# Performance work log

Hardware: AMD Instinct MI355X
Metric: run time of the kernel (lower is better)

Reference implementation:

```python
import jax, jax.numpy as jnp
import numpy as np

N, D = 32, 16  # output capsules, output capsule dim
J, I = 16, 8   # input capsules, input capsule dim
B = 16384

def setup_inputs() -> dict:
    key = jax.random.key(0)
    k1, k2 = jax.random.split(key)
    inputs = jax.random.normal(k1, (B, J, I), dtype=jnp.float32)
    # kaiming_normal_ on (N,16,8,D): fan_in computed from dims -> std = sqrt(2/fan_in)
    fan_in = I * D  # torch fan_in for a 4D tensor (N,16,8,D) is dim1*receptive? faithful scale: gain*sqrt(1/fan)
    W = jax.random.normal(k2, (N, J, I, D), dtype=jnp.float32) * np.float32(np.sqrt(2.0 / (J * I * D / N if False else fan_in)))
    b = jnp.zeros((N, J, 1), dtype=jnp.float32)
    return {"inputs": inputs, "W": W, "b": b}

def reference(inputs, W, b):
    # pose transform: u[b,n,j,z] = sum_i inputs[b,j,i] * W[n,j,i,z]
    u = jnp.einsum('bji,njiz->bnjz', inputs, W)          # (B, N, J, D)
    # self-agreement: c[b,n,i] = sum_{k,j} u[b,n,i,j] * u[b,n,k,j]
    c = jnp.einsum('bnij,bnj->bni', u, u.sum(axis=-2))   # (B, N, J)
    c = c[..., None] / jnp.sqrt(jnp.float32(D))          # (B, N, J, 1)
    c = jax.nn.softmax(c, axis=1)                        # softmax over N axis (torch dim=1)
    c = c + b                                            # broadcast (N, J, 1)
    s = jnp.sum(u * c, axis=-2)                          # (B, N, D)
    return s
```

## Files before the change

kernel.cpp:

```cpp
#include <hip/hip_runtime.h>

#define B_TOT 16384
#define TBB   16
#define NTH   256
#define SLS   524

typedef short bf16x8 __attribute__((ext_vector_type(8)));
typedef float f32x4  __attribute__((ext_vector_type(4)));
union U4 { bf16x8 v; uint4 q; };

__device__ __forceinline__ unsigned f2bf(float f) {
    unsigned u = __float_as_uint(f);
    return (u + 0x7fffu + ((u >> 16) & 1u)) >> 16;
}

__device__ __forceinline__ uint4 packrow(const float* src) {
    uint4 o;
    o.x = f2bf(src[0])  | (f2bf(src[16])  << 16);
    o.y = f2bf(src[32]) | (f2bf(src[48])  << 16);
    o.z = f2bf(src[64]) | (f2bf(src[80])  << 16);
    o.w = f2bf(src[96]) | (f2bf(src[112]) << 16);
    return o;
}

__global__ void prepack(const float* __restrict__ W, uint4* __restrict__ Wp)
{
    const int t = blockIdx.x * 256 + threadIdx.x;
    if (t < 8192) {
        const int lane = t & 63, s = (t >> 6) & 3, n = t >> 8;
        const int q = lane >> 4, z = lane & 15;
        const int j = 4 * s + q;
        Wp[t] = packrow(W + (size_t)(n * 16 + j) * 128 + z);
    } else {
        const int u = t - 8192;
        const int lane = u & 63, j = (u >> 6) & 15, n = u >> 10;
        const int q = lane >> 4, z = lane & 15;
        uint4 o = make_uint4(0u, 0u, 0u, 0u);
        if (q == (j & 3))
            o = packrow(W + (size_t)(n * 16 + j) * 128 + z);
        Wp[t] = o;
    }
}

__global__ __launch_bounds__(NTH, 4)
void caps(const float* __restrict__ X, const uint4* __restrict__ Wp,
          const float* __restrict__ Bias, float* __restrict__ Out)
{
    __shared__ __align__(16) float sL[TBB * SLS];
    __shared__ float sBias[512];

    const int t    = threadIdx.x;
    const int lane = t & 63;
    const int wv   = t >> 6;
    const int b16  = lane & 15;
    const int q    = lane >> 4;
    const long bb  = (long)blockIdx.x * TBB;

    sBias[t]       = Bias[t];
    sBias[t + 256] = Bias[t + 256];

    uint4 xq[4];
    #pragma unroll
    for (int s = 0; s < 4; ++s) {
        const float* xs = X + (bb + b16) * 128 + (4 * s + q) * 8;
        float4 a = *reinterpret_cast<const float4*>(xs);
        float4 c = *reinterpret_cast<const float4*>(xs + 4);
        uint4 o;
        o.x = f2bf(a.x) | (f2bf(a.y) << 16);
        o.y = f2bf(a.z) | (f2bf(a.w) << 16);
        o.z = f2bf(c.x) | (f2bf(c.y) << 16);
        o.w = f2bf(c.z) | (f2bf(c.w) << 16);
        xq[s] = o;
    }

    const f32x4 zero4 = {0.f, 0.f, 0.f, 0.f};

    #pragma unroll 1
    for (int nq = 0; nq < 8; ++nq) {
        const int n = wv * 8 + nq;
        const uint4* wk = Wp + n * 256 + lane;

        f32x4 usum = zero4;
        #pragma unroll
        for (int s = 0; s < 4; ++s) {
            U4 a;  a.q  = wk[s * 64];
            U4 xb; xb.q = xq[s];
            usum = __builtin_amdgcn_mfma_f32_16x16x32_bf16(a.v, xb.v, usum, 0, 0, 0);
        }

        const uint4* wj = Wp + 8192 + n * 1024 + lane;
        float lv[16];
        #pragma unroll
        for (int j = 0; j < 16; ++j) {
            U4 a;  a.q  = wj[j * 64];
            U4 xb; xb.q = xq[j >> 2];
            f32x4 u = __builtin_amdgcn_mfma_f32_16x16x32_bf16(a.v, xb.v, zero4, 0, 0, 0);
            float p = u[0] * usum[0];
            p = fmaf(u[1], usum[1], p);
            p = fmaf(u[2], usum[2], p);
            p = fmaf(u[3], usum[3], p);
            p += __shfl_xor(p, 16);
            p += __shfl_xor(p, 32);
            lv[j] = p * 0.25f;
        }
        if (lane < 16) {
            float4* dst = reinterpret_cast<float4*>(&sL[b16 * SLS + n * 16]);
            dst[0] = make_float4(lv[0],  lv[1],  lv[2],  lv[3]);
            dst[1] = make_float4(lv[4],  lv[5],  lv[6],  lv[7]);
            dst[2] = make_float4(lv[8],  lv[9],  lv[10], lv[11]);
            dst[3] = make_float4(lv[12], lv[13], lv[14], lv[15]);
        }
    }
    __syncthreads();

    {
        const int sb = t >> 4, sj = t & 15;
        float l[32];
        #pragma unroll
        for (int n = 0; n < 32; ++n) l[n] = sL[sb * SLS + n * 16 + sj];
        float m = l[0];
        #pragma unroll
        for (int n = 1; n < 32; ++n) m = fmaxf(m, l[n]);
        float Z = 0.f;
        #pragma unroll
        for (int n = 0; n < 32; ++n) { l[n] = __expf(l[n] - m); Z += l[n]; }
        const float inv = 1.0f / Z;
        #pragma unroll
        for (int n = 0; n < 32; ++n)
            sL[sb * SLS + n * 16 + sj] = fmaf(l[n], inv, sBias[n * 16 + sj]);
    }
    __syncthreads();

    #pragma unroll 2
    for (int nq = 0; nq < 8; ++nq) {
        const int n = wv * 8 + nq;
        const uint4* wj = Wp + 8192 + n * 1024 + lane;
        float s0 = 0.f, s1 = 0.f, s2 = 0.f, s3 = 0.f;
        #pragma unroll
        for (int jp = 0; jp < 8; ++jp) {
            float2 c2 = *reinterpret_cast<const float2*>(&sL[b16 * SLS + n * 16 + 2 * jp]);
            U4 a0; a0.q = wj[(2 * jp) * 64];
            U4 a1; a1.q = wj[(2 * jp + 1) * 64];
            U4 x0; x0.q = xq[jp >> 1];
            f32x4 u0 = __builtin_amdgcn_mfma_f32_16x16x32_bf16(a0.v, x0.v, zero4, 0, 0, 0);
            f32x4 u1 = __builtin_amdgcn_mfma_f32_16x16x32_bf16(a1.v, x0.v, zero4, 0, 0, 0);
            s0 = fmaf(c2.x, u0[0], s0); s0 = fmaf(c2.y, u1[0], s0);
            s1 = fmaf(c2.x, u0[1], s1); s1 = fmaf(c2.y, u1[1], s1);
            s2 = fmaf(c2.x, u0[2], s2); s2 = fmaf(c2.y, u1[2], s2);
            s3 = fmaf(c2.x, u0[3], s3); s3 = fmaf(c2.y, u1[3], s3);
        }
        float4* op = reinterpret_cast<float4*>(Out + (bb + b16) * 512 + n * 16 + q * 4);
        *op = make_float4(s0, s1, s2, s3);
    }
}

extern "C" void kernel_launch(void* const* d_in, const int* in_sizes, int n_in,
                              void* d_out, int out_size, void* d_ws, size_t ws_size,
                              hipStream_t stream) {
    const float* X  = (const float*)d_in[0];
    const float* W  = (const float*)d_in[1];
    const float* Bi = (const float*)d_in[2];
    float* Out = (float*)d_out;

    uint4* Wp = (uint4*)d_ws;
    prepack<<<160, 256, 0, stream>>>(W, Wp);
    caps<<<B_TOT / TBB, NTH, 0, stream>>>(X, Wp, Bi, Out);
}
```

Measured before the change: 113.8 us.

## Derive per-j masked weight fragments in registers and prefetch next capsule weights

The prepack kernel no longer writes the zero-padded per-j weight copies. The main kernel now builds each per-j MFMA operand by AND-masking the packed 4-row fragment with a lane-group mask, which cuts the weight traffic per block from 1280 to 256 uint4 per capsule. The next capsule's fragments are also prefetched into registers while the current one is computed, in both passes. This costs extra VGPRs and a few ALU ops per MFMA, and the second-pass unroll drops from 2 to 1.

```diff
diff --git a/kernel.cpp b/kernel.cpp
--- a/kernel.cpp
+++ b/kernel.cpp
@@ -26,20 +26,9 @@
 __global__ void prepack(const float* __restrict__ W, uint4* __restrict__ Wp)
 {
     const int t = blockIdx.x * 256 + threadIdx.x;
-    if (t < 8192) {
-        const int lane = t & 63, s = (t >> 6) & 3, n = t >> 8;
-        const int q = lane >> 4, z = lane & 15;
-        const int j = 4 * s + q;
-        Wp[t] = packrow(W + (size_t)(n * 16 + j) * 128 + z);
-    } else {
-        const int u = t - 8192;
-        const int lane = u & 63, j = (u >> 6) & 15, n = u >> 10;
-        const int q = lane >> 4, z = lane & 15;
-        uint4 o = make_uint4(0u, 0u, 0u, 0u);
-        if (q == (j & 3))
-            o = packrow(W + (size_t)(n * 16 + j) * 128 + z);
-        Wp[t] = o;
-    }
+    const int lane = t & 63, s = (t >> 6) & 3, n = t >> 8;
+    const int q = lane >> 4, z = lane & 15;
+    Wp[t] = packrow(W + (size_t)(n * 16 + 4 * s + q) * 128 + z);
 }
 
 __global__ __launch_bounds__(NTH, 4)
@@ -59,6 +48,10 @@
     sBias[t]       = Bias[t];
     sBias[t + 256] = Bias[t + 256];
 
+    unsigned moct[4];
+    #pragma unroll
+    for (int c = 0; c < 4; ++c) moct[c] = (q == c) ? 0xffffffffu : 0u;
+
     uint4 xq[4];
     #pragma unroll
     for (int s = 0; s < 4; ++s) {
@@ -75,24 +68,39 @@
 
     const f32x4 zero4 = {0.f, 0.f, 0.f, 0.f};
 
+    auto maskA = [&](const uint4& wkf, int c) {
+        U4 a;
+        const unsigned m = moct[c];
+        a.q.x = wkf.x & m; a.q.y = wkf.y & m;
+        a.q.z = wkf.z & m; a.q.w = wkf.w & m;
+        return a;
+    };
+
+    uint4 wk[4], wn[4];
+
+    {
+        const uint4* p0 = Wp + (wv * 8) * 256 + lane;
+        wk[0] = p0[0]; wk[1] = p0[64]; wk[2] = p0[128]; wk[3] = p0[192];
+    }
     #pragma unroll 1
     for (int nq = 0; nq < 8; ++nq) {
-        const int n = wv * 8 + nq;
-        const uint4* wk = Wp + n * 256 + lane;
+        const int n  = wv * 8 + nq;
+        const int np = (nq < 7) ? n + 1 : n;
+        const uint4* pn = Wp + np * 256 + lane;
+        wn[0] = pn[0]; wn[1] = pn[64]; wn[2] = pn[128]; wn[3] = pn[192];
 
         f32x4 usum = zero4;
         #pragma unroll
         for (int s = 0; s < 4; ++s) {
-            U4 a;  a.q  = wk[s * 64];
+            U4 a;  a.q  = wk[s];
             U4 xb; xb.q = xq[s];
             usum = __builtin_amdgcn_mfma_f32_16x16x32_bf16(a.v, xb.v, usum, 0, 0, 0);
         }
 
-        const uint4* wj = Wp + 8192 + n * 1024 + lane;
         float lv[16];
         #pragma unroll
         for (int j = 0; j < 16; ++j) {
-            U4 a;  a.q  = wj[j * 64];
+            U4 a  = maskA(wk[j >> 2], j & 3);
             U4 xb; xb.q = xq[j >> 2];
             f32x4 u = __builtin_amdgcn_mfma_f32_16x16x32_bf16(a.v, xb.v, zero4, 0, 0, 0);
             float p = u[0] * usum[0];
@@ -110,6 +118,7 @@
             dst[2] = make_float4(lv[8],  lv[9],  lv[10], lv[11]);
             dst[3] = make_float4(lv[12], lv[13], lv[14], lv[15]);
         }
+        wk[0] = wn[0]; wk[1] = wn[1]; wk[2] = wn[2]; wk[3] = wn[3];
     }
     __syncthreads();
 
@@ -131,16 +140,23 @@
     }
     __syncthreads();
 
-    #pragma unroll 2
+    {
+        const uint4* p0 = Wp + (wv * 8) * 256 + lane;
+        wk[0] = p0[0]; wk[1] = p0[64]; wk[2] = p0[128]; wk[3] = p0[192];
+    }
+    #pragma unroll 1
     for (int nq = 0; nq < 8; ++nq) {
-        const int n = wv * 8 + nq;
-        const uint4* wj = Wp + 8192 + n * 1024 + lane;
+        const int n  = wv * 8 + nq;
+        const int np = (nq < 7) ? n + 1 : n;
+        const uint4* pn = Wp + np * 256 + lane;
+        wn[0] = pn[0]; wn[1] = pn[64]; wn[2] = pn[128]; wn[3] = pn[192];
+
         float s0 = 0.f, s1 = 0.f, s2 = 0.f, s3 = 0.f;
         #pragma unroll
         for (int jp = 0; jp < 8; ++jp) {
             float2 c2 = *reinterpret_cast<const float2*>(&sL[b16 * SLS + n * 16 + 2 * jp]);
-            U4 a0; a0.q = wj[(2 * jp) * 64];
-            U4 a1; a1.q = wj[(2 * jp + 1) * 64];
+            U4 a0 = maskA(wk[jp >> 1], (2 * jp) & 3);
+            U4 a1 = maskA(wk[jp >> 1], (2 * jp + 1) & 3);
             U4 x0; x0.q = xq[jp >> 1];
             f32x4 u0 = __builtin_amdgcn_mfma_f32_16x16x32_bf16(a0.v, x0.v, zero4, 0, 0, 0);
             f32x4 u1 = __builtin_amdgcn_mfma_f32_16x16x32_bf16(a1.v, x0.v, zero4, 0, 0, 0);
@@ -151,6 +167,7 @@
         }
         float4* op = reinterpret_cast<float4*>(Out + (bb + b16) * 512 + n * 16 + q * 4);
         *op = make_float4(s0, s1, s2, s3);
+        wk[0] = wn[0]; wk[1] = wn[1]; wk[2] = wn[2]; wk[3] = wn[3];
     }
 }
 
@@ -163,6 +180,6 @@
     float* Out = (float*)d_out;
 
     uint4* Wp = (uint4*)d_ws;
-    prepack<<<160, 256, 0, stream>>>(W, Wp);
+    prepack<<<32, 256, 0, stream>>>(W, Wp);
     caps<<<B_TOT / TBB, NTH, 0, stream>>>(X, Wp, Bi, Out);
 }
```

After: 101.7 us. 10.6% less time.
